# Kernel tuning notes

Measured on AMD Instinct MI355X. Metric: run time of the kernel, lower is better.

## Reference

```python
import jax, jax.numpy as jnp
import numpy as np

EPS = 1e-5   # torch nn.LayerNorm default
H = 12       # num_heads


def layernorm(x, w, b):
    m = jnp.mean(x, axis=-1, keepdims=True)
    v = jnp.var(x, axis=-1, keepdims=True)
    return (x - m) * jax.lax.rsqrt(v + EPS) * w + b


def mha(x, qkv_w, proj_w, proj_b):
    # MemEffAttention math (qkv_bias=False, proj_bias=True), block-diagonal mask
    # over equal-length sequences == independent per-row attention.
    B, N, D = x.shape
    hd = D // H
    qkv = jnp.einsum('bnd,ed->bne', x, qkv_w).reshape(B, N, 3, H, hd)
    q, k, v = qkv[:, :, 0], qkv[:, :, 1], qkv[:, :, 2]
    scale = hd ** -0.5
    attn = jnp.einsum('bnhd,bmhd->bhnm', q * scale, k)     # [B,H,N,N]
    attn = jax.nn.softmax(attn, axis=-1)
    o = jnp.einsum('bhnm,bmhd->bnhd', attn, v).reshape(B, N, D)
    return jnp.einsum('bnd,ed->bne', o, proj_w) + proj_b


def block(x, ln1_w, ln1_b, qkv_w, proj_w, proj_b, ln2_w, ln2_b, fc1_w, fc1_b, fc2_w, fc2_b):
    # x = x + attn(norm1(x)); x = x + mlp(norm2(x))  (ls1/ls2 = Identity, eval mode)
    x = x + mha(layernorm(x, ln1_w, ln1_b), qkv_w, proj_w, proj_b)
    h = layernorm(x, ln2_w, ln2_b)
    h = jax.nn.gelu(jnp.einsum('bnd,ed->bne', h, fc1_w) + fc1_b, approximate=False)
    h = jnp.einsum('bne,de->bnd', h, fc2_w) + fc2_b
    return x + h


def setup_inputs() -> dict:
    key = jax.random.key(0)
    ks = jax.random.split(key, 8)
    D, Dff = 768, 3072
    s = lambda k, shape, sc: jax.random.normal(k, shape, jnp.float32) * sc
    return {
        'x1': s(ks[0], (8, 1370, D), 1.0),
        'x2': s(ks[1], (8, 257, D), 1.0),
        'ln1_w': jnp.ones((D,), jnp.float32), 'ln1_b': jnp.zeros((D,), jnp.float32),
        'qkv_w': s(ks[2], (3 * D, D), 0.02),
        'proj_w': s(ks[3], (D, D), 0.02), 'proj_b': jnp.zeros((D,), jnp.float32),
        'ln2_w': jnp.ones((D,), jnp.float32), 'ln2_b': jnp.zeros((D,), jnp.float32),
        'fc1_w': s(ks[4], (Dff, D), 0.02), 'fc1_b': jnp.zeros((Dff,), jnp.float32),
        'fc2_w': s(ks[5], (D, Dff), 0.02), 'fc2_b': jnp.zeros((D,), jnp.float32),
    }


def reference(x1, x2, ln1_w, ln1_b, qkv_w, proj_w, proj_b, ln2_w, ln2_b,
              fc1_w, fc1_b, fc2_w, fc2_b):
    # forward_nested (eval path): block-diagonal attention over nested groups,
    # which factorizes into per-group batched attention; return the
    # concatenated token stream (same values as attn_bias.split output).
    params = (ln1_w, ln1_b, qkv_w, proj_w, proj_b, ln2_w, ln2_b,
              fc1_w, fc1_b, fc2_w, fc2_b)
    o1 = block(x1, *params)
    o2 = block(x2, *params)
    D = x1.shape[-1]
    return jnp.concatenate([o1.reshape(-1, D), o2.reshape(-1, D)], axis=0)
```

## Files before the change

### kernel.cpp

```cpp
#include <hip/hip_runtime.h>
#include <hip/hip_bf16.h>

typedef __attribute__((ext_vector_type(8))) short bf16x8;
typedef __attribute__((ext_vector_type(4))) float f32x4;
typedef __attribute__((ext_vector_type(16))) float f32x16;

#define GL_LDS16(g, l)                                                        \
  __builtin_amdgcn_global_load_lds((const __attribute__((address_space(1))) void*)(g), \
                                   (__attribute__((address_space(3))) void*)(l), 16, 0, 0)

__device__ __forceinline__ ushort f2bf(float f) {
  union { float f; unsigned u; } x; x.f = f;
  unsigned r = x.u + 0x7fffu + ((x.u >> 16) & 1u);
  return (ushort)(r >> 16);
}

__device__ __forceinline__ float max3f(float a, float b, float c) {
  float d;
  asm("v_max3_f32 %0, %1, %2, %3" : "=v"(d) : "v"(a), "v"(b), "v"(c));
  return d;
}

__device__ __forceinline__ int xcd_remap(int bid, int nwg) {
  int q = nwg >> 3, r = nwg & 7;
  int xcd = bid & 7, idx = bid >> 3;
  return (xcd < r ? xcd * (q + 1) : r * (q + 1) + (xcd - r) * q) + idx;
}

__global__ void cvt4_kernel(const float* __restrict__ i0, const float* __restrict__ i1,
                            const float* __restrict__ i2, const float* __restrict__ i3,
                            int n0, int n1, int n2, int n3,
                            ushort* __restrict__ out) {
  int c1 = n0, c2 = n0 + n1, c3 = n0 + n1 + n2, nt = n0 + n1 + n2 + n3;
  int i = blockIdx.x * blockDim.x + threadIdx.x;
  int stride = gridDim.x * blockDim.x;
  for (; i < nt; i += stride) {
    float v;
    if (i < c1) v = i0[i];
    else if (i < c2) v = i1[i - c1];
    else if (i < c3) v = i2[i - c2];
    else v = i3[i - c3];
    out[i] = f2bf(v);
  }
}

__global__ __launch_bounds__(256) void ln_kernel(
    const float* __restrict__ x1, const float* __restrict__ x2, int M1, int MT,
    const float* __restrict__ w, const float* __restrict__ b,
    ushort* __restrict__ out) {
  int row = blockIdx.x * 4 + (threadIdx.x >> 6);
  if (row >= MT) return;
  int lane = threadIdx.x & 63;
  const float* xr = (row < M1) ? x1 + (size_t)row * 768
                               : x2 + (size_t)(row - M1) * 768;
  float4 v[3];
  float s = 0.f, sq = 0.f;
#pragma unroll
  for (int i = 0; i < 3; i++) {
    v[i] = *(const float4*)(xr + i * 256 + lane * 4);
    s += v[i].x + v[i].y + v[i].z + v[i].w;
    sq += v[i].x * v[i].x + v[i].y * v[i].y + v[i].z * v[i].z + v[i].w * v[i].w;
  }
#pragma unroll
  for (int m = 1; m < 64; m <<= 1) { s += __shfl_xor(s, m); sq += __shfl_xor(sq, m); }
  float mean = s * (1.f / 768.f);
  float var = sq * (1.f / 768.f) - mean * mean;
  float rstd = rsqrtf(var + 1e-5f);
  ushort* orow = out + (size_t)row * 768;
#pragma unroll
  for (int i = 0; i < 3; i++) {
    int d = i * 256 + lane * 4;
    float4 wv = *(const float4*)(w + d);
    float4 bv = *(const float4*)(b + d);
    ushort4 o;
    o.x = f2bf((v[i].x - mean) * rstd * wv.x + bv.x);
    o.y = f2bf((v[i].y - mean) * rstd * wv.y + bv.y);
    o.z = f2bf((v[i].z - mean) * rstd * wv.z + bv.z);
    o.w = f2bf((v[i].w - mean) * rstd * wv.w + bv.w);
    *(ushort4*)(orow + d) = o;
  }
}

template <int MODE>
__global__ __launch_bounds__(256) void gemm_tile(
    const ushort* __restrict__ A, const ushort* __restrict__ W,
    const float* __restrict__ bias, void* __restrict__ outp,
    int M, int N, int K, int ncol) {
  __shared__ ushort lA[128 * 64];
  __shared__ ushort lB[128 * 64];
  const int t = threadIdx.x;
  const int lane = t & 63, wave = t >> 6;
  const int l15 = lane & 15, lg = lane >> 4;
  const int waveM = wave >> 1, waveN = wave & 1;
  const int g = xcd_remap(blockIdx.x, gridDim.x);
  const int rowBlk = (g / ncol) * 128;
  const int colBlk = (g % ncol) * 128;
  const int srow = t >> 3;
  const int schunk = t & 7;

  f32x4 acc[4][4] = {};

  for (int k0 = 0; k0 < K; k0 += 64) {
    if (k0) __syncthreads();
#pragma unroll
    for (int i = 0; i < 4; i++) {
      int row = i * 32 + srow;
      int gch = schunk ^ (row & 7);
      GL_LDS16(A + (size_t)(rowBlk + row) * K + k0 + gch * 8,
               &lA[row * 64 + schunk * 8]);
      GL_LDS16(W + (size_t)(colBlk + row) * K + k0 + gch * 8,
               &lB[row * 64 + schunk * 8]);
    }
    __syncthreads();
#pragma unroll
    for (int kk = 0; kk < 2; kk++) {
      bf16x8 af[4], bfr[4];
#pragma unroll
      for (int m = 0; m < 4; m++) {
        int row = waveM * 64 + m * 16 + l15;
        af[m] = *(const bf16x8*)&lA[row * 64 + ((kk * 32 + lg * 8) ^ ((row & 7) << 3))];
      }
#pragma unroll
      for (int c = 0; c < 4; c++) {
        int row = waveN * 64 + c * 16 + l15;
        bfr[c] = *(const bf16x8*)&lB[row * 64 + ((kk * 32 + lg * 8) ^ ((row & 7) << 3))];
      }
      __builtin_amdgcn_s_setprio(1);
#pragma unroll
      for (int m = 0; m < 4; m++)
#pragma unroll
        for (int c = 0; c < 4; c++)
          acc[m][c] = __builtin_amdgcn_mfma_f32_16x16x32_bf16(af[m], bfr[c], acc[m][c], 0, 0, 0);
      __builtin_amdgcn_s_setprio(0);
    }
  }

  const float qsc = (MODE == 0 && colBlk < 768) ? 0.18033688011112042f : 1.f;
#pragma unroll
  for (int m = 0; m < 4; m++) {
    int rowB = rowBlk + waveM * 64 + m * 16 + lg * 4;
#pragma unroll
    for (int c = 0; c < 4; c++) {
      int col = colBlk + waveN * 64 + c * 16 + l15;
      float bv = (MODE == 2) ? bias[col] : 0.f;
#pragma unroll
      for (int j = 0; j < 4; j++) {
        int r = rowB + j;
        if (r < M) {
          float v = acc[m][c][j] + bv;
          size_t idx = (size_t)r * N + col;
          if (MODE == 2) {
            float gl = 0.5f * v * (1.f + erff(v * 0.70710678118f));
            ((ushort*)outp)[idx] = f2bf(gl);
          } else {
            ((ushort*)outp)[idx] = f2bf(v * qsc);
          }
        }
      }
    }
  }
}

__global__ __launch_bounds__(256) void gemm_tile64(
    const ushort* __restrict__ A, const ushort* __restrict__ W,
    const float* __restrict__ bias, const float* __restrict__ res1,
    const float* __restrict__ res2, int resSplit,
    float* __restrict__ outp, int M, int N, int K, int ncol) {
  __shared__ ushort lA[64 * 64];
  __shared__ ushort lB[128 * 64];
  const int t = threadIdx.x;
  const int lane = t & 63, wave = t >> 6;
  const int l15 = lane & 15, lg = lane >> 4;
  const int waveM = wave >> 1, waveN = wave & 1;
  const int g = xcd_remap(blockIdx.x, gridDim.x);
  const int rowBlk = (g / ncol) * 64;
  const int colBlk = (g % ncol) * 128;
  const int srow = t >> 3;
  const int schunk = t & 7;

  f32x4 acc[2][4] = {};

  for (int k0 = 0; k0 < K; k0 += 64) {
    if (k0) __syncthreads();
#pragma unroll
    for (int i = 0; i < 2; i++) {
      int row = i * 32 + srow;
      int gch = schunk ^ (row & 7);
      GL_LDS16(A + (size_t)(rowBlk + row) * K + k0 + gch * 8,
               &lA[row * 64 + schunk * 8]);
    }
#pragma unroll
    for (int i = 0; i < 4; i++) {
      int row = i * 32 + srow;
      int gch = schunk ^ (row & 7);
      GL_LDS16(W + (size_t)(colBlk + row) * K + k0 + gch * 8,
               &lB[row * 64 + schunk * 8]);
    }
    __syncthreads();
#pragma unroll
    for (int kk = 0; kk < 2; kk++) {
      bf16x8 af[2], bfr[4];
#pragma unroll
      for (int m = 0; m < 2; m++) {
        int row = waveM * 32 + m * 16 + l15;
        af[m] = *(const bf16x8*)&lA[row * 64 + ((kk * 32 + lg * 8) ^ ((row & 7) << 3))];
      }
#pragma unroll
      for (int c = 0; c < 4; c++) {
        int row = waveN * 64 + c * 16 + l15;
        bfr[c] = *(const bf16x8*)&lB[row * 64 + ((kk * 32 + lg * 8) ^ ((row & 7) << 3))];
      }
      __builtin_amdgcn_s_setprio(1);
#pragma unroll
      for (int m = 0; m < 2; m++)
#pragma unroll
        for (int c = 0; c < 4; c++)
          acc[m][c] = __builtin_amdgcn_mfma_f32_16x16x32_bf16(af[m], bfr[c], acc[m][c], 0, 0, 0);
      __builtin_amdgcn_s_setprio(0);
    }
  }

#pragma unroll
  for (int m = 0; m < 2; m++) {
    int rowB = rowBlk + waveM * 32 + m * 16 + lg * 4;
#pragma unroll
    for (int c = 0; c < 4; c++) {
      int col = colBlk + waveN * 64 + c * 16 + l15;
      float bv = bias[col];
#pragma unroll
      for (int j = 0; j < 4; j++) {
        int r = rowB + j;
        if (r < M) {
          size_t idx = (size_t)r * N + col;
          float rv = (r < resSplit) ? res1[idx]
                                    : res2[(size_t)(r - resSplit) * N + col];
          outp[idx] = acc[m][c][j] + bv + rv;
        }
      }
    }
  }
}

__global__ __launch_bounds__(256) void prep_kernel(
    const ushort* __restrict__ qkv, ushort* __restrict__ kt2,
    ushort* __restrict__ vt2, int N1, int N2, int nkv1, int nkv2, int M1) {
  __shared__ ushort lT[64 * 68];
  const int t = threadIdx.x;
  const int bhg = blockIdx.x;
  const int kv = blockIdx.y;
  const int part = bhg >= 96;
  const int bh = part ? bhg - 96 : bhg;
  const int N = part ? N2 : N1;
  const int nkv = part ? nkv2 : nkv1;
  if (kv >= nkv) return;
  const size_t rowbase = part ? (size_t)M1 : 0;
  const int b = bh / 12, h = bh % 12;
  const int k0 = kv * 64;
  const ushort* Kp = qkv + (rowbase + (size_t)b * N) * 2304 + 768 + h * 64;
  const ushort* Vp = Kp + 768;
  size_t tbase = (part ? (size_t)96 * nkv1 : 0) + (size_t)bh * nkv + kv;
  ushort* ktile = kt2 + tbase * 4096;
  ushort* vtile = vt2 + tbase * 4096;
#pragma unroll
  for (int p = 0; p < 2; p++) {
    int s = p * 256 + t;
    int chunk = s >> 6, krow = s & 63;
    ushort4 v0 = {0, 0, 0, 0}, v1 = {0, 0, 0, 0};
    if (k0 + krow < N) {
      const ushort* src = Kp + (size_t)(k0 + krow) * 2304 + chunk * 8;
      v0 = *(const ushort4*)src;
      v1 = *(const ushort4*)(src + 4);
    }
    *(ushort4*)&ktile[s * 8] = v0;
    *(ushort4*)&ktile[s * 8 + 4] = v1;
  }
#pragma unroll
  for (int p = 0; p < 2; p++) {
    int nl = p * 32 + (t >> 3);
    int dc = t & 7;
    ushort4 v0 = {0, 0, 0, 0}, v1 = {0, 0, 0, 0};
    if (k0 + nl < N) {
      const ushort* src = Vp + (size_t)(k0 + nl) * 2304 + dc * 8;
      v0 = *(const ushort4*)src;
      v1 = *(const ushort4*)(src + 4);
    }
    *(ushort4*)&lT[nl * 68 + dc * 8] = v0;
    *(ushort4*)&lT[nl * 68 + dc * 8 + 4] = v1;
  }
  __syncthreads();
#pragma unroll
  for (int p = 0; p < 2; p++) {
    int s = p * 256 + t;
    int kchunk = s >> 6, d = s & 63;
    ushort o[8];
#pragma unroll
    for (int j = 0; j < 8; j++) o[j] = lT[(kchunk * 8 + j) * 68 + d];
    *(ushort4*)&vtile[s * 8] = *(ushort4*)o;
    *(ushort4*)&vtile[s * 8 + 4] = *(ushort4*)(o + 4);
  }
}

#define ATTN_STAGE(buf, kvi)                                                   \
  do {                                                                         \
    _Pragma("unroll") for (int p = 0; p < 2; p++) {                            \
      int s = p * 256 + t;                                                     \
      GL_LDS16(tK + (size_t)(kvi) * 4096 + s * 8, &lK[buf][s * 8]);            \
      GL_LDS16(tV + (size_t)(kvi) * 4096 + s * 8, &lV[buf][s * 8]);            \
    }                                                                          \
  } while (0)

__global__ __launch_bounds__(256) void attn_kernel(
    const ushort* __restrict__ qkv, const ushort* __restrict__ kt2,
    const ushort* __restrict__ vt2, ushort* __restrict__ o_out,
    int N1, int N2, int nkv1, int nkv2, int M1) {
  __shared__ ushort lK[2][4096];
  __shared__ ushort lV[2][4096];
  const int t = threadIdx.x;
  const int lane = t & 63, wave = t >> 6;
  const int l31 = lane & 31, hi = lane >> 5;
  const int bhg = blockIdx.x;
  const int part = bhg >= 96;
  const int bh = part ? bhg - 96 : bhg;
  const int N = part ? N2 : N1;
  const int nkv = part ? nkv2 : nkv1;
  const int qb = blockIdx.y * 128;
  if (qb >= N) return;
  const size_t rowbase = part ? (size_t)M1 : 0;
  const int b = bh / 12, h = bh % 12;
  const ushort* Qp = qkv + (rowbase + (size_t)b * N) * 2304 + h * 64;
  const size_t tboff = (part ? (size_t)96 * nkv1 : 0) + (size_t)bh * nkv;
  const ushort* tK = kt2 + tboff * 4096;
  const ushort* tV = vt2 + tboff * 4096;

  const int qrow = min(qb + wave * 32 + l31, N - 1);
  bf16x8 qf[4];
#pragma unroll
  for (int kc = 0; kc < 4; kc++)
    qf[kc] = *(const bf16x8*)(Qp + (size_t)qrow * 2304 + kc * 16 + hi * 8);

  union { unsigned u[4]; bf16x8 v; } ones;
#pragma unroll
  for (int i = 0; i < 4; i++) ones.u[i] = 0x3F803F80u;

  f32x16 oacc[2] = {};
  f32x16 osum = {};
  float mrun = -1e30f;

  ATTN_STAGE(0, 0);
  __syncthreads();
  for (int kv = 0; kv < nkv; kv++) {
    int cur = kv & 1;
    if (kv + 1 < nkv) ATTN_STAGE(cur ^ 1, kv + 1);
    const bool fullTile = (kv * 64 + 64 <= N);
    f32x16 sacc0 = {}, sacc1 = {};
    __builtin_amdgcn_s_setprio(1);
#pragma unroll
    for (int kc = 0; kc < 4; kc++) {
      bf16x8 kf0 = *(const bf16x8*)&lK[cur][(((kc * 2 + hi) << 6) + l31) * 8];
      bf16x8 kf1 = *(const bf16x8*)&lK[cur][(((kc * 2 + hi) << 6) + 32 + l31) * 8];
      sacc0 = __builtin_amdgcn_mfma_f32_32x32x16_bf16(kf0, qf[kc], sacc0, 0, 0, 0);
      sacc1 = __builtin_amdgcn_mfma_f32_32x32x16_bf16(kf1, qf[kc], sacc1, 0, 0, 0);
    }
    __builtin_amdgcn_s_setprio(0);
    float z[32];
#pragma unroll
    for (int r = 0; r < 16; r++) { z[r] = sacc0[r]; z[16 + r] = sacc1[r]; }
    if (!fullTile) {
#pragma unroll
      for (int i = 0; i < 32; i++) {
        int kg = kv * 64 + (i >> 4) * 32 + (i & 3) + (((i & 15) >> 2) << 3) + (hi << 2);
        if (kg >= N) z[i] = -1e30f;
      }
    }
    float mA[11];
#pragma unroll
    for (int i = 0; i < 10; i++) mA[i] = max3f(z[3 * i], z[3 * i + 1], z[3 * i + 2]);
    mA[10] = fmaxf(z[30], z[31]);
    float mB[4];
#pragma unroll
    for (int i = 0; i < 3; i++) mB[i] = max3f(mA[3 * i], mA[3 * i + 1], mA[3 * i + 2]);
    mB[3] = fmaxf(mA[9], mA[10]);
    float mx = fmaxf(max3f(mB[0], mB[1], mB[2]), mB[3]);
    {
      float a = mx, bx = mx;
      asm("v_permlane32_swap_b32 %0, %1" : "+&v"(a), "+v"(bx));
      mx = fmaxf(a, bx);
    }
    if (!__all(mx <= mrun + 8.f)) {
      float mnew = fmaxf(mrun, mx);
      float corr = exp2f(mrun - mnew);
      oacc[0] *= corr;
      oacc[1] *= corr;
      osum *= corr;
      mrun = mnew;
    }
#pragma unroll
    for (int i = 0; i < 32; i++) z[i] = exp2f(z[i] - mrun);
#pragma unroll
    for (int kt = 0; kt < 2; kt++) {
      unsigned w0[4], w1[4];
#pragma unroll
      for (int rr = 0; rr < 4; rr++) {
        asm("v_cvt_pk_bf16_f32 %0, %1, %2" : "=v"(w0[rr]) : "v"(z[kt * 16 + 4 * rr]), "v"(z[kt * 16 + 4 * rr + 1]));
        asm("v_cvt_pk_bf16_f32 %0, %1, %2" : "=v"(w1[rr]) : "v"(z[kt * 16 + 4 * rr + 2]), "v"(z[kt * 16 + 4 * rr + 3]));
      }
#pragma unroll
      for (int kc2 = 0; kc2 < 2; kc2++) {
        unsigned ua = w0[2 * kc2], ub = w0[2 * kc2 + 1];
        unsigned uc = w1[2 * kc2], ud = w1[2 * kc2 + 1];
        asm("v_permlane32_swap_b32 %0, %1" : "+&v"(ua), "+v"(ub));
        asm("v_permlane32_swap_b32 %0, %1" : "+&v"(uc), "+v"(ud));
        union { unsigned u[4]; bf16x8 v; } pa;
        pa.u[0] = ua; pa.u[1] = uc; pa.u[2] = ub; pa.u[3] = ud;
        int kcg = kt * 2 + kc2;
        __builtin_amdgcn_s_setprio(1);
#pragma unroll
        for (int dt = 0; dt < 2; dt++) {
          bf16x8 vf = *(const bf16x8*)&lV[cur][(((kcg * 2 + hi) << 6) + dt * 32 + l31) * 8];
          oacc[dt] = __builtin_amdgcn_mfma_f32_32x32x16_bf16(pa.v, vf, oacc[dt], 0, 0, 0);
        }
        osum = __builtin_amdgcn_mfma_f32_32x32x16_bf16(pa.v, ones.v, osum, 0, 0, 0);
        __builtin_amdgcn_s_setprio(0);
      }
    }
    __syncthreads();
  }
#pragma unroll
  for (int r = 0; r < 16; r++) {
    int q = qb + wave * 32 + (r & 3) + ((r >> 2) << 3) + (hi << 2);
    if (q < N) {
      float inv;
      asm("v_rcp_f32 %0, %1" : "=v"(inv) : "v"(osum[r]));
      ushort* orow = o_out + (rowbase + (size_t)b * N + q) * 768 + h * 64;
      orow[l31] = f2bf(oacc[0][r] * inv);
      orow[32 + l31] = f2bf(oacc[1][r] * inv);
    }
  }
}

extern "C" void kernel_launch(void* const* d_in, const int* in_sizes, int n_in,
                              void* d_out, int out_size, void* d_ws, size_t ws_size,
                              hipStream_t stream) {
  const float* x1 = (const float*)d_in[0];
  const float* x2 = (const float*)d_in[1];
  const float* ln1_w = (const float*)d_in[2];
  const float* ln1_b = (const float*)d_in[3];
  const float* qkv_w = (const float*)d_in[4];
  const float* proj_w = (const float*)d_in[5];
  const float* proj_b = (const float*)d_in[6];
  const float* ln2_w = (const float*)d_in[7];
  const float* ln2_b = (const float*)d_in[8];
  const float* fc1_w = (const float*)d_in[9];
  const float* fc1_b = (const float*)d_in[10];
  const float* fc2_w = (const float*)d_in[11];
  const float* fc2_b = (const float*)d_in[12];
  float* out = (float*)d_out;

  const int N1 = 1370, N2 = 257;
  const int M1 = 8 * N1, M2 = 8 * N2;
  const int MT = M1 + M2;
  const int MPAD = 13056;
  const int nkv1 = 22, nkv2 = 5;

  char* ws = (char*)d_ws;
  ushort* wq = (ushort*)ws;   ws += (size_t)2304 * 768 * 2;
  ushort* wp = (ushort*)ws;   ws += (size_t)768 * 768 * 2;
  ushort* w1 = (ushort*)ws;   ws += (size_t)3072 * 768 * 2;
  ushort* w2 = (ushort*)ws;   ws += (size_t)768 * 3072 * 2;
  ushort* bufA = (ushort*)ws;   ws += (size_t)MPAD * 768 * 2;
  ushort* bufQKV = (ushort*)ws; ws += (size_t)MPAD * 2304 * 2;
  ushort* bufFF = (ushort*)ws;  ws += (size_t)MPAD * 3072 * 2;
  const size_t nTiles = (size_t)96 * (nkv1 + nkv2);
  ushort* kt2 = bufFF;
  ushort* vt2 = bufFF + nTiles * 4096;

  cvt4_kernel<<<2048, 256, 0, stream>>>(qkv_w, proj_w, fc1_w, fc2_w,
                                        2304 * 768, 768 * 768, 3072 * 768, 768 * 3072, wq);

  ln_kernel<<<(MT + 3) / 4, 256, 0, stream>>>(x1, x2, M1, MT, ln1_w, ln1_b, bufA);
  gemm_tile<0><<<(MPAD / 128) * 18, 256, 0, stream>>>(
      bufA, wq, nullptr, bufQKV, MT, 2304, 768, 18);
  prep_kernel<<<dim3(192, nkv1), 256, 0, stream>>>(bufQKV, kt2, vt2, N1, N2, nkv1, nkv2, M1);
  attn_kernel<<<dim3(192, 11), 256, 0, stream>>>(
      bufQKV, kt2, vt2, bufA, N1, N2, nkv1, nkv2, M1);
  gemm_tile64<<<(MPAD / 64) * 6, 256, 0, stream>>>(
      bufA, wp, proj_b, x1, x2, M1, out, MT, 768, 768, 6);
  ln_kernel<<<(MT + 3) / 4, 256, 0, stream>>>(out, out, MT, MT, ln2_w, ln2_b, bufA);
  gemm_tile<2><<<(MPAD / 128) * 24, 256, 0, stream>>>(
      bufA, w1, fc1_b, bufFF, MT, 3072, 768, 24);
  gemm_tile64<<<(MPAD / 64) * 6, 256, 0, stream>>>(
      bufFF, w2, fc2_b, out, nullptr, MT, out, MT, 768, 3072, 6);
}
```

Baseline: 479.3 us.

## Double-buffer GEMM LDS tiles with vmcnt-gated prefetch and k-chunk-major layout

Both GEMM kernels now use two LDS buffers. The next K-tile is issued with global_load_lds while the current tile is consumed, and progress is gated with explicit s_waitcnt vmcnt plus barriers instead of full __syncthreads around each load. The LDS layout changes from XOR-swizzled row-major to k-chunk-major (chunk, row), so MFMA fragment reads are contiguous per chunk. The 128x128 kernel also shrinks its K-step to 32 so the double buffer fits in the same LDS. This is meant to hide global load latency behind MFMA work, at the cost of more barriers per K and possible LDS bank conflicts from the unswizzled layout.

```diff
diff --git a/kernel.cpp b/kernel.cpp
--- a/kernel.cpp
+++ b/kernel.cpp
@@ -8,6 +8,19 @@
 #define GL_LDS16(g, l)                                                        \
   __builtin_amdgcn_global_load_lds((const __attribute__((address_space(1))) void*)(g), \
                                    (__attribute__((address_space(3))) void*)(l), 16, 0, 0)
+
+#define WAIT_VM(N)                                                             \
+  do {                                                                         \
+    asm volatile("s_waitcnt vmcnt(" #N ")" ::: "memory");                      \
+    __builtin_amdgcn_s_barrier();                                              \
+    __builtin_amdgcn_sched_barrier(0);                                         \
+  } while (0)
+#define WAIT_LGKM()                                                            \
+  do {                                                                         \
+    asm volatile("s_waitcnt lgkmcnt(0)" ::: "memory");                         \
+    __builtin_amdgcn_s_barrier();                                              \
+    __builtin_amdgcn_sched_barrier(0);                                         \
+  } while (0)
 
 __device__ __forceinline__ ushort f2bf(float f) {
   union { float f; unsigned u; } x; x.f = f;
@@ -81,13 +94,38 @@
   }
 }
 
+#define GT_STG(buf, tstep)                                                     \
+  do {                                                                         \
+    int k0s = (tstep) << 5;                                                    \
+    _Pragma("unroll") for (int p = 0; p < 2; p++) {                            \
+      int s = p * 256 + t;                                                     \
+      int ch = s >> 7, rw = s & 127;                                           \
+      GL_LDS16(A + (size_t)(rowBlk + rw) * K + k0s + ch * 8, &lA[buf][s * 8]); \
+      GL_LDS16(W + (size_t)(colBlk + rw) * K + k0s + ch * 8, &lB[buf][s * 8]); \
+    }                                                                          \
+  } while (0)
+
+#define GT_COMPUTE(cbuf)                                                       \
+  do {                                                                         \
+    bf16x8 af[4], bfr[4];                                                      \
+    _Pragma("unroll") for (int m = 0; m < 4; m++)                              \
+      af[m] = *(const bf16x8*)&lA[cbuf][(lg * 128 + waveM * 64 + m * 16 + l15) * 8]; \
+    _Pragma("unroll") for (int cc = 0; cc < 4; cc++)                           \
+      bfr[cc] = *(const bf16x8*)&lB[cbuf][(lg * 128 + waveN * 64 + cc * 16 + l15) * 8]; \
+    __builtin_amdgcn_s_setprio(1);                                             \
+    _Pragma("unroll") for (int m = 0; m < 4; m++)                              \
+      _Pragma("unroll") for (int cc = 0; cc < 4; cc++)                         \
+        acc[m][cc] = __builtin_amdgcn_mfma_f32_16x16x32_bf16(af[m], bfr[cc], acc[m][cc], 0, 0, 0); \
+    __builtin_amdgcn_s_setprio(0);                                             \
+  } while (0)
+
 template <int MODE>
 __global__ __launch_bounds__(256) void gemm_tile(
     const ushort* __restrict__ A, const ushort* __restrict__ W,
     const float* __restrict__ bias, void* __restrict__ outp,
     int M, int N, int K, int ncol) {
-  __shared__ ushort lA[128 * 64];
-  __shared__ ushort lB[128 * 64];
+  __shared__ ushort lA[2][128 * 32];
+  __shared__ ushort lB[2][128 * 32];
   const int t = threadIdx.x;
   const int lane = t & 63, wave = t >> 6;
   const int l15 = lane & 15, lg = lane >> 4;
@@ -95,45 +133,20 @@
   const int g = xcd_remap(blockIdx.x, gridDim.x);
   const int rowBlk = (g / ncol) * 128;
   const int colBlk = (g % ncol) * 128;
-  const int srow = t >> 3;
-  const int schunk = t & 7;
 
   f32x4 acc[4][4] = {};
-
-  for (int k0 = 0; k0 < K; k0 += 64) {
-    if (k0) __syncthreads();
-#pragma unroll
-    for (int i = 0; i < 4; i++) {
-      int row = i * 32 + srow;
-      int gch = schunk ^ (row & 7);
-      GL_LDS16(A + (size_t)(rowBlk + row) * K + k0 + gch * 8,
-               &lA[row * 64 + schunk * 8]);
-      GL_LDS16(W + (size_t)(colBlk + row) * K + k0 + gch * 8,
-               &lB[row * 64 + schunk * 8]);
-    }
-    __syncthreads();
-#pragma unroll
-    for (int kk = 0; kk < 2; kk++) {
-      bf16x8 af[4], bfr[4];
-#pragma unroll
-      for (int m = 0; m < 4; m++) {
-        int row = waveM * 64 + m * 16 + l15;
-        af[m] = *(const bf16x8*)&lA[row * 64 + ((kk * 32 + lg * 8) ^ ((row & 7) << 3))];
-      }
-#pragma unroll
-      for (int c = 0; c < 4; c++) {
-        int row = waveN * 64 + c * 16 + l15;
-        bfr[c] = *(const bf16x8*)&lB[row * 64 + ((kk * 32 + lg * 8) ^ ((row & 7) << 3))];
-      }
-      __builtin_amdgcn_s_setprio(1);
-#pragma unroll
-      for (int m = 0; m < 4; m++)
-#pragma unroll
-        for (int c = 0; c < 4; c++)
-          acc[m][c] = __builtin_amdgcn_mfma_f32_16x16x32_bf16(af[m], bfr[c], acc[m][c], 0, 0, 0);
-      __builtin_amdgcn_s_setprio(0);
-    }
-  }
+  const int nt = K >> 5;
+
+  GT_STG(0, 0);
+  for (int tt = 0; tt < nt - 1; ++tt) {
+    const int c = tt & 1;
+    GT_STG(c ^ 1, tt + 1);
+    WAIT_VM(4);
+    GT_COMPUTE(c);
+    WAIT_LGKM();
+  }
+  WAIT_VM(0);
+  GT_COMPUTE((nt - 1) & 1);
 
   const float qsc = (MODE == 0 && colBlk < 768) ? 0.18033688011112042f : 1.f;
 #pragma unroll
@@ -161,13 +174,44 @@
   }
 }
 
+#define G64_STG(buf, tstep)                                                    \
+  do {                                                                         \
+    int k0s = (tstep) << 6;                                                    \
+    _Pragma("unroll") for (int p = 0; p < 2; p++) {                            \
+      int s = p * 256 + t;                                                     \
+      int ch = s >> 6, rw = s & 63;                                            \
+      GL_LDS16(A + (size_t)(rowBlk + rw) * K + k0s + ch * 8, &lA[buf][s * 8]); \
+    }                                                                          \
+    _Pragma("unroll") for (int p = 0; p < 4; p++) {                            \
+      int s = p * 256 + t;                                                     \
+      int ch = s >> 7, rw = s & 127;                                           \
+      GL_LDS16(W + (size_t)(colBlk + rw) * K + k0s + ch * 8, &lB[buf][s * 8]); \
+    }                                                                          \
+  } while (0)
+
+#define G64_COMPUTE(cbuf)                                                      \
+  do {                                                                         \
+    _Pragma("unroll") for (int kk = 0; kk < 2; kk++) {                         \
+      bf16x8 af[2], bfr[4];                                                    \
+      _Pragma("unroll") for (int m = 0; m < 2; m++)                            \
+        af[m] = *(const bf16x8*)&lA[cbuf][((kk * 4 + lg) * 64 + waveM * 32 + m * 16 + l15) * 8]; \
+      _Pragma("unroll") for (int cc = 0; cc < 4; cc++)                         \
+        bfr[cc] = *(const bf16x8*)&lB[cbuf][((kk * 4 + lg) * 128 + waveN * 64 + cc * 16 + l15) * 8]; \
+      __builtin_amdgcn_s_setprio(1);                                           \
+      _Pragma("unroll") for (int m = 0; m < 2; m++)                            \
+        _Pragma("unroll") for (int cc = 0; cc < 4; cc++)                       \
+          acc[m][cc] = __builtin_amdgcn_mfma_f32_16x16x32_bf16(af[m], bfr[cc], acc[m][cc], 0, 0, 0); \
+      __builtin_amdgcn_s_setprio(0);                                           \
+    }                                                                          \
+  } while (0)
+
 __global__ __launch_bounds__(256) void gemm_tile64(
     const ushort* __restrict__ A, const ushort* __restrict__ W,
     const float* __restrict__ bias, const float* __restrict__ res1,
     const float* __restrict__ res2, int resSplit,
     float* __restrict__ outp, int M, int N, int K, int ncol) {
-  __shared__ ushort lA[64 * 64];
-  __shared__ ushort lB[128 * 64];
+  __shared__ ushort lA[2][64 * 64];
+  __shared__ ushort lB[2][128 * 64];
   const int t = threadIdx.x;
   const int lane = t & 63, wave = t >> 6;
   const int l15 = lane & 15, lg = lane >> 4;
@@ -175,50 +219,20 @@
   const int g = xcd_remap(blockIdx.x, gridDim.x);
   const int rowBlk = (g / ncol) * 64;
   const int colBlk = (g % ncol) * 128;
-  const int srow = t >> 3;
-  const int schunk = t & 7;
 
   f32x4 acc[2][4] = {};
-
-  for (int k0 = 0; k0 < K; k0 += 64) {
-    if (k0) __syncthreads();
-#pragma unroll
-    for (int i = 0; i < 2; i++) {
-      int row = i * 32 + srow;
-      int gch = schunk ^ (row & 7);
-      GL_LDS16(A + (size_t)(rowBlk + row) * K + k0 + gch * 8,
-               &lA[row * 64 + schunk * 8]);
-    }
-#pragma unroll
-    for (int i = 0; i < 4; i++) {
-      int row = i * 32 + srow;
-      int gch = schunk ^ (row & 7);
-      GL_LDS16(W + (size_t)(colBlk + row) * K + k0 + gch * 8,
-               &lB[row * 64 + schunk * 8]);
-    }
-    __syncthreads();
-#pragma unroll
-    for (int kk = 0; kk < 2; kk++) {
-      bf16x8 af[2], bfr[4];
-#pragma unroll
-      for (int m = 0; m < 2; m++) {
-        int row = waveM * 32 + m * 16 + l15;
-        af[m] = *(const bf16x8*)&lA[row * 64 + ((kk * 32 + lg * 8) ^ ((row & 7) << 3))];
-      }
-#pragma unroll
-      for (int c = 0; c < 4; c++) {
-        int row = waveN * 64 + c * 16 + l15;
-        bfr[c] = *(const bf16x8*)&lB[row * 64 + ((kk * 32 + lg * 8) ^ ((row & 7) << 3))];
-      }
-      __builtin_amdgcn_s_setprio(1);
-#pragma unroll
-      for (int m = 0; m < 2; m++)
-#pragma unroll
-        for (int c = 0; c < 4; c++)
-          acc[m][c] = __builtin_amdgcn_mfma_f32_16x16x32_bf16(af[m], bfr[c], acc[m][c], 0, 0, 0);
-      __builtin_amdgcn_s_setprio(0);
-    }
-  }
+  const int nt = K >> 6;
+
+  G64_STG(0, 0);
+  for (int tt = 0; tt < nt - 1; ++tt) {
+    const int c = tt & 1;
+    G64_STG(c ^ 1, tt + 1);
+    WAIT_VM(6);
+    G64_COMPUTE(c);
+    WAIT_LGKM();
+  }
+  WAIT_VM(0);
+  G64_COMPUTE((nt - 1) & 1);
 
 #pragma unroll
   for (int m = 0; m < 2; m++) {
```

New measurement: 746.9 us. 1.56x slower.
